# Optimization experiments

Measured on AMD Instinct MI355X. Metric: run time of the kernel, lower is better.

The kernel has to match this reference:

```python
import jax, jax.numpy as jnp
import numpy as np

TAU = 2.0         # LIFNode default tau
VTH = 1.0         # v_threshold
ALPHA = 2.0       # ATan surrogate alpha
TIME_STEP = 4     # hard-coded in RecurrentLIFNode
NUM_LAYERS = 4
HIDDEN = 512
INPUT = 512
T, B = 128, 512

@jax.custom_vjp
def atan_spike(x):
    # heaviside forward, ATan surrogate backward (spikingjelly surrogate.ATan)
    return (x >= 0.0).astype(x.dtype)

def _atan_fwd(x):
    return atan_spike(x), x

def _atan_bwd(x, g):
    return (g * (ALPHA / 2.0) / (1.0 + (jnp.pi / 2.0 * ALPHA * x) ** 2),)

atan_spike.defvjp(_atan_fwd, _atan_bwd)

def lif_burst(v, inp):
    # run one LIFCell time_step times with fixed input `inp`, accumulate averages
    acc_v = jnp.zeros_like(v)
    acc_s = jnp.zeros_like(v)
    for _ in range(TIME_STEP):
        v = v + (inp - v) / TAU          # neuronal_charge (decay_input=True, v_reset=None)
        s = atan_spike(v - VTH)          # neuronal_fire
        v = v - s * VTH                  # soft reset (v_reset=None)
        acc_v = acc_v + v
        acc_s = acc_s + s
    return v, acc_v / TIME_STEP, acc_s / TIME_STEP


def setup_inputs() -> dict:
    key = jax.random.key(0)
    k1, k2, k3 = jax.random.split(key, 3)
    x = jax.random.normal(k1, (T, B, INPUT), dtype=jnp.float32)
    bound = 1.0 / np.sqrt(INPUT)
    W = jax.random.uniform(k2, (HIDDEN, INPUT), dtype=jnp.float32, minval=-bound, maxval=bound)
    b = jax.random.uniform(k3, (HIDDEN,), dtype=jnp.float32, minval=-bound, maxval=bound)
    return {"x": x, "W": W, "b": b}


def reference(x, W, b):
    # x: [T, B, input]; project once (linear_ih)
    xp = jnp.einsum('tbi,hi->tbh', x, W) + b   # [T, B, H]
    Bsz, H = x.shape[1], W.shape[0]
    init_state = jnp.zeros((NUM_LAYERS, Bsz, H), dtype=x.dtype)  # current_state persists across t

    def step(cur, xt):
        curs = [cur[i] for i in range(NUM_LAYERS)]
        y = xt
        new_vs = []
        last_spk = None
        for i in range(NUM_LAYERS):
            curs[i], avg_v, avg_s = lif_burst(curs[i], y)
            new_vs.append(avg_v)
            y = avg_v          # next layer consumes averaged membrane state
            last_spk = avg_s
        return jnp.stack(curs), (last_spk, jnp.stack(new_vs))

    _, (out, states_seq) = jax.lax.scan(step, init_state, xp)
    # out: [T, B, H] averaged spikes of last layer; final new_states_list: [L, B, H]
    return out, states_seq[-1]
```

## Files before the change

kernel.cpp:

```cpp
#include <hip/hip_runtime.h>
#include <stdint.h>

#define TT 128
#define BSZ 512
#define HID 512
#define KDIM 512
#define BH (BSZ*HID)

__global__ __launch_bounds__(256) void gemm_f32(
    const float* __restrict__ A, const float* __restrict__ W,
    const float* __restrict__ bias, float* __restrict__ C) {
  __shared__ float As[2][16][132];
  __shared__ float Bs[2][16][132];
  const int t  = threadIdx.x;
  const int m0 = blockIdx.y * 128;
  const int n0 = blockIdx.x * 128;
  const int tx = t & 15;
  const int ty = t >> 4;
  const int r0 = t >> 2;
  const int kg = t & 3;

  float acc[8][8];
  #pragma unroll
  for (int i = 0; i < 8; ++i)
    #pragma unroll
    for (int j = 0; j < 8; ++j) acc[i][j] = 0.f;

  const float* Ap = A + (size_t)(m0 + r0) * KDIM + kg * 4;
  const float* Wp = W + (size_t)(n0 + r0) * KDIM + kg * 4;

  float4 a0 = *(const float4*)Ap;
  float4 w0 = *(const float4*)Wp;
  float4 a1 = *(const float4*)(Ap + (size_t)64 * KDIM);
  float4 w1 = *(const float4*)(Wp + (size_t)64 * KDIM);

  #define STAGE(BUF) do { \
    As[BUF][kg*4+0][r0]    = a0.x; As[BUF][kg*4+1][r0]    = a0.y; \
    As[BUF][kg*4+2][r0]    = a0.z; As[BUF][kg*4+3][r0]    = a0.w; \
    Bs[BUF][kg*4+0][r0]    = w0.x; Bs[BUF][kg*4+1][r0]    = w0.y; \
    Bs[BUF][kg*4+2][r0]    = w0.z; Bs[BUF][kg*4+3][r0]    = w0.w; \
    As[BUF][kg*4+0][r0+64] = a1.x; As[BUF][kg*4+1][r0+64] = a1.y; \
    As[BUF][kg*4+2][r0+64] = a1.z; As[BUF][kg*4+3][r0+64] = a1.w; \
    Bs[BUF][kg*4+0][r0+64] = w1.x; Bs[BUF][kg*4+1][r0+64] = w1.y; \
    Bs[BUF][kg*4+2][r0+64] = w1.z; Bs[BUF][kg*4+3][r0+64] = w1.w; \
  } while (0)

  STAGE(0);

  int cur = 0;
  for (int k0 = 0; k0 < KDIM; k0 += 16) {
    __syncthreads();
    const bool more = (k0 + 16 < KDIM);
    if (more) {
      a0 = *(const float4*)(Ap + k0 + 16);
      w0 = *(const float4*)(Wp + k0 + 16);
      a1 = *(const float4*)(Ap + (size_t)64 * KDIM + k0 + 16);
      w1 = *(const float4*)(Wp + (size_t)64 * KDIM + k0 + 16);
    }

    #pragma unroll
    for (int kk = 0; kk < 16; ++kk) {
      const float4 xa0 = *(const float4*)&As[cur][kk][ty*8];
      const float4 xa1 = *(const float4*)&As[cur][kk][ty*8 + 4];
      const float4 xb0 = *(const float4*)&Bs[cur][kk][tx*4];
      const float4 xb1 = *(const float4*)&Bs[cur][kk][64 + tx*4];
      const float a[8] = {xa0.x,xa0.y,xa0.z,xa0.w,xa1.x,xa1.y,xa1.z,xa1.w};
      const float b[8] = {xb0.x,xb0.y,xb0.z,xb0.w,xb1.x,xb1.y,xb1.z,xb1.w};
      #pragma unroll
      for (int i = 0; i < 8; ++i)
        #pragma unroll
        for (int j = 0; j < 8; ++j)
          acc[i][j] = __builtin_fmaf(a[i], b[j], acc[i][j]);
    }

    if (more) {
      const int nb = cur ^ 1;
      STAGE(nb);
    }
    cur ^= 1;
  }
  #undef STAGE

  const float4 bv0 = *(const float4*)&bias[n0 + tx*4];
  const float4 bv1 = *(const float4*)&bias[n0 + 64 + tx*4];
  #pragma unroll
  for (int i = 0; i < 8; ++i) {
    const float4 v0 = {acc[i][0] + bv0.x, acc[i][1] + bv0.y, acc[i][2] + bv0.z, acc[i][3] + bv0.w};
    const float4 v1 = {acc[i][4] + bv1.x, acc[i][5] + bv1.y, acc[i][6] + bv1.z, acc[i][7] + bv1.w};
    float* cp = C + (size_t)(m0 + ty*8 + i) * HID + n0;
    *(float4*)(cp + tx*4)      = v0;
    *(float4*)(cp + 64 + tx*4) = v1;
  }
}

__device__ __forceinline__ float lif_step(float y, float v[4], float av[4]) {
  float as3 = 0.f;
  #pragma unroll
  for (int l = 0; l < 4; ++l) {
    float vv = v[l];
    float accv = 0.f, accs = 0.f;
    #pragma unroll
    for (int k = 0; k < 4; ++k) {
      const float d = y - vv;
      vv = __builtin_fmaf(d, 0.5f, vv);
      const float spk = (vv >= 1.0f) ? 1.0f : 0.0f;
      vv -= spk;
      accv += vv;
      accs += spk;
    }
    v[l] = vv;
    const float a = accv * 0.25f;
    av[l] = a;
    y = a;
    as3 = accs;
  }
  return as3;
}

__global__ __launch_bounds__(256) void lif_scan(
    const float* __restrict__ xp, float* __restrict__ outp, float* __restrict__ vstate,
    int tc, int first, int last) {
  const int idx = blockIdx.x * 256 + threadIdx.x;
  float v[4];
  if (first) {
    #pragma unroll
    for (int l = 0; l < 4; ++l) v[l] = 0.f;
  } else {
    #pragma unroll
    for (int l = 0; l < 4; ++l) v[l] = vstate[(size_t)l * BH + idx];
  }
  float av[4] = {0.f, 0.f, 0.f, 0.f};
  const float* p = xp + idx;
  float* op = outp + idx;

  if ((tc & 3) == 0 && tc >= 8) {
    float curb[4];
    #pragma unroll
    for (int i = 0; i < 4; ++i) curb[i] = p[(size_t)i * BH];
    for (int t = 0; t + 4 < tc; t += 4) {
      float nxtb[4];
      #pragma unroll
      for (int i = 0; i < 4; ++i) nxtb[i] = p[(size_t)(i + 4) * BH];
      #pragma unroll
      for (int i = 0; i < 4; ++i) {
        const float as3 = lif_step(curb[i], v, av);
        op[(size_t)i * BH] = as3 * 0.25f;
      }
      #pragma unroll
      for (int i = 0; i < 4; ++i) curb[i] = nxtb[i];
      p += 4 * BH; op += 4 * BH;
    }
    #pragma unroll
    for (int i = 0; i < 4; ++i) {
      const float as3 = lif_step(curb[i], v, av);
      op[(size_t)i * BH] = as3 * 0.25f;
    }
  } else {
    for (int t = 0; t < tc; ++t) {
      const float as3 = lif_step(p[0], v, av);
      *op = as3 * 0.25f;
      p += BH; op += BH;
    }
  }

  if (last) {
    #pragma unroll
    for (int l = 0; l < 4; ++l) vstate[(size_t)l * BH + idx] = av[l];
  } else {
    #pragma unroll
    for (int l = 0; l < 4; ++l) vstate[(size_t)l * BH + idx] = v[l];
  }
}

extern "C" void kernel_launch(void* const* d_in, const int* in_sizes, int n_in,
                              void* d_out, int out_size, void* d_ws, size_t ws_size,
                              hipStream_t stream) {
  const float* x = (const float*)d_in[0];
  const float* W = (const float*)d_in[1];
  const float* b = (const float*)d_in[2];
  float* out    = (float*)d_out;
  float* states = out + (size_t)TT * BH;

  int tc = TT;
  while (tc > 1 && (size_t)tc * BH * 4ull > ws_size) tc >>= 1;
  float* xp = (float*)d_ws;
  const int nc = TT / tc;

  for (int c = 0; c < nc; ++c) {
    hipLaunchKernelGGL(gemm_f32, dim3(HID / 128, tc * BSZ / 128), dim3(256), 0, stream,
                       x + (size_t)c * tc * BH, W, b, xp);
    hipLaunchKernelGGL(lif_scan, dim3(BH / 256), dim3(256), 0, stream,
                       xp, out + (size_t)c * tc * BH, states,
                       tc, c == 0 ? 1 : 0, c == nc - 1 ? 1 : 0);
  }
}
```

Baseline: 615.9 us.

## Enlarge GEMM tile to 256x128 and process two elements per thread in LIF scan

The FP32 GEMM tile grows from 128x128 to 256x128, so each thread computes a 16x8 accumulator block, with four A rows staged per thread and launch bounds raised to two blocks per CU. This raises arithmetic intensity per shared-memory load and halves the grid. The LIF scan now handles two neighbouring elements per thread using float2 loads and stores, which gives each thread two independent dependency chains to interleave. The cost is much higher register pressure in the GEMM (128 accumulators), which could spill or reduce occupancy, and half as many threads in the scan.

After: 710.0 us. 15.3% more time.

```diff
diff --git a/kernel.cpp b/kernel.cpp
--- a/kernel.cpp
+++ b/kernel.cpp
@@ -7,45 +7,56 @@
 #define KDIM 512
 #define BH (BSZ*HID)
 
-__global__ __launch_bounds__(256) void gemm_f32(
+__global__ __launch_bounds__(256, 2) void gemm_f32(
     const float* __restrict__ A, const float* __restrict__ W,
     const float* __restrict__ bias, float* __restrict__ C) {
-  __shared__ float As[2][16][132];
+  __shared__ float As[2][16][260];
   __shared__ float Bs[2][16][132];
   const int t  = threadIdx.x;
-  const int m0 = blockIdx.y * 128;
+  const int m0 = blockIdx.y * 256;
   const int n0 = blockIdx.x * 128;
   const int tx = t & 15;
   const int ty = t >> 4;
   const int r0 = t >> 2;
-  const int kg = t & 3;
-
-  float acc[8][8];
+  const int kg4 = (t & 3) * 4;
+
+  float4 acc0[16], acc1[16];
   #pragma unroll
-  for (int i = 0; i < 8; ++i)
-    #pragma unroll
-    for (int j = 0; j < 8; ++j) acc[i][j] = 0.f;
-
-  const float* Ap = A + (size_t)(m0 + r0) * KDIM + kg * 4;
-  const float* Wp = W + (size_t)(n0 + r0) * KDIM + kg * 4;
+  for (int i = 0; i < 16; ++i) {
+    acc0[i] = (float4){0.f,0.f,0.f,0.f};
+    acc1[i] = (float4){0.f,0.f,0.f,0.f};
+  }
+
+  const float* Ap = A + (size_t)(m0 + r0) * KDIM + kg4;
+  const float* Wp = W + (size_t)(n0 + r0) * KDIM + kg4;
 
   float4 a0 = *(const float4*)Ap;
+  float4 a1 = *(const float4*)(Ap + (size_t)64  * KDIM);
+  float4 a2 = *(const float4*)(Ap + (size_t)128 * KDIM);
+  float4 a3 = *(const float4*)(Ap + (size_t)192 * KDIM);
   float4 w0 = *(const float4*)Wp;
-  float4 a1 = *(const float4*)(Ap + (size_t)64 * KDIM);
   float4 w1 = *(const float4*)(Wp + (size_t)64 * KDIM);
 
   #define STAGE(BUF) do { \
-    As[BUF][kg*4+0][r0]    = a0.x; As[BUF][kg*4+1][r0]    = a0.y; \
-    As[BUF][kg*4+2][r0]    = a0.z; As[BUF][kg*4+3][r0]    = a0.w; \
-    Bs[BUF][kg*4+0][r0]    = w0.x; Bs[BUF][kg*4+1][r0]    = w0.y; \
-    Bs[BUF][kg*4+2][r0]    = w0.z; Bs[BUF][kg*4+3][r0]    = w0.w; \
-    As[BUF][kg*4+0][r0+64] = a1.x; As[BUF][kg*4+1][r0+64] = a1.y; \
-    As[BUF][kg*4+2][r0+64] = a1.z; As[BUF][kg*4+3][r0+64] = a1.w; \
-    Bs[BUF][kg*4+0][r0+64] = w1.x; Bs[BUF][kg*4+1][r0+64] = w1.y; \
-    Bs[BUF][kg*4+2][r0+64] = w1.z; Bs[BUF][kg*4+3][r0+64] = w1.w; \
+    As[BUF][kg4+0][r0]     = a0.x; As[BUF][kg4+1][r0]     = a0.y; As[BUF][kg4+2][r0]     = a0.z; As[BUF][kg4+3][r0]     = a0.w; \
+    As[BUF][kg4+0][r0+64]  = a1.x; As[BUF][kg4+1][r0+64]  = a1.y; As[BUF][kg4+2][r0+64]  = a1.z; As[BUF][kg4+3][r0+64]  = a1.w; \
+    As[BUF][kg4+0][r0+128] = a2.x; As[BUF][kg4+1][r0+128] = a2.y; As[BUF][kg4+2][r0+128] = a2.z; As[BUF][kg4+3][r0+128] = a2.w; \
+    As[BUF][kg4+0][r0+192] = a3.x; As[BUF][kg4+1][r0+192] = a3.y; As[BUF][kg4+2][r0+192] = a3.z; As[BUF][kg4+3][r0+192] = a3.w; \
+    Bs[BUF][kg4+0][r0]     = w0.x; Bs[BUF][kg4+1][r0]     = w0.y; Bs[BUF][kg4+2][r0]     = w0.z; Bs[BUF][kg4+3][r0]     = w0.w; \
+    Bs[BUF][kg4+0][r0+64]  = w1.x; Bs[BUF][kg4+1][r0+64]  = w1.y; Bs[BUF][kg4+2][r0+64]  = w1.z; Bs[BUF][kg4+3][r0+64]  = w1.w; \
   } while (0)
 
   STAGE(0);
+
+  #define FMA8(AV, I) \
+    acc0[I].x = __builtin_fmaf(AV, bf0.x, acc0[I].x); \
+    acc0[I].y = __builtin_fmaf(AV, bf0.y, acc0[I].y); \
+    acc0[I].z = __builtin_fmaf(AV, bf0.z, acc0[I].z); \
+    acc0[I].w = __builtin_fmaf(AV, bf0.w, acc0[I].w); \
+    acc1[I].x = __builtin_fmaf(AV, bf1.x, acc1[I].x); \
+    acc1[I].y = __builtin_fmaf(AV, bf1.y, acc1[I].y); \
+    acc1[I].z = __builtin_fmaf(AV, bf1.z, acc1[I].z); \
+    acc1[I].w = __builtin_fmaf(AV, bf1.w, acc1[I].w);
 
   int cur = 0;
   for (int k0 = 0; k0 < KDIM; k0 += 16) {
@@ -53,41 +64,40 @@
     const bool more = (k0 + 16 < KDIM);
     if (more) {
       a0 = *(const float4*)(Ap + k0 + 16);
+      a1 = *(const float4*)(Ap + (size_t)64  * KDIM + k0 + 16);
+      a2 = *(const float4*)(Ap + (size_t)128 * KDIM + k0 + 16);
+      a3 = *(const float4*)(Ap + (size_t)192 * KDIM + k0 + 16);
       w0 = *(const float4*)(Wp + k0 + 16);
-      a1 = *(const float4*)(Ap + (size_t)64 * KDIM + k0 + 16);
       w1 = *(const float4*)(Wp + (size_t)64 * KDIM + k0 + 16);
     }
 
     #pragma unroll
     for (int kk = 0; kk < 16; ++kk) {
-      const float4 xa0 = *(const float4*)&As[cur][kk][ty*8];
-      const float4 xa1 = *(const float4*)&As[cur][kk][ty*8 + 4];
-      const float4 xb0 = *(const float4*)&Bs[cur][kk][tx*4];
-      const float4 xb1 = *(const float4*)&Bs[cur][kk][64 + tx*4];
-      const float a[8] = {xa0.x,xa0.y,xa0.z,xa0.w,xa1.x,xa1.y,xa1.z,xa1.w};
-      const float b[8] = {xb0.x,xb0.y,xb0.z,xb0.w,xb1.x,xb1.y,xb1.z,xb1.w};
-      #pragma unroll
-      for (int i = 0; i < 8; ++i)
-        #pragma unroll
-        for (int j = 0; j < 8; ++j)
-          acc[i][j] = __builtin_fmaf(a[i], b[j], acc[i][j]);
-    }
-
-    if (more) {
-      const int nb = cur ^ 1;
-      STAGE(nb);
-    }
+      const float4 bf0 = *(const float4*)&Bs[cur][kk][tx*4];
+      const float4 bf1 = *(const float4*)&Bs[cur][kk][64 + tx*4];
+      const float4 af0 = *(const float4*)&As[cur][kk][ty*16];
+      const float4 af1 = *(const float4*)&As[cur][kk][ty*16 + 4];
+      const float4 af2 = *(const float4*)&As[cur][kk][ty*16 + 8];
+      const float4 af3 = *(const float4*)&As[cur][kk][ty*16 + 12];
+      FMA8(af0.x, 0)  FMA8(af0.y, 1)  FMA8(af0.z, 2)  FMA8(af0.w, 3)
+      FMA8(af1.x, 4)  FMA8(af1.y, 5)  FMA8(af1.z, 6)  FMA8(af1.w, 7)
+      FMA8(af2.x, 8)  FMA8(af2.y, 9)  FMA8(af2.z, 10) FMA8(af2.w, 11)
+      FMA8(af3.x, 12) FMA8(af3.y, 13) FMA8(af3.z, 14) FMA8(af3.w, 15)
+    }
+
+    if (more) STAGE(cur ^ 1);
     cur ^= 1;
   }
   #undef STAGE
+  #undef FMA8
 
   const float4 bv0 = *(const float4*)&bias[n0 + tx*4];
   const float4 bv1 = *(const float4*)&bias[n0 + 64 + tx*4];
   #pragma unroll
-  for (int i = 0; i < 8; ++i) {
-    const float4 v0 = {acc[i][0] + bv0.x, acc[i][1] + bv0.y, acc[i][2] + bv0.z, acc[i][3] + bv0.w};
-    const float4 v1 = {acc[i][4] + bv1.x, acc[i][5] + bv1.y, acc[i][6] + bv1.z, acc[i][7] + bv1.w};
-    float* cp = C + (size_t)(m0 + ty*8 + i) * HID + n0;
+  for (int i = 0; i < 16; ++i) {
+    const float4 v0 = {acc0[i].x + bv0.x, acc0[i].y + bv0.y, acc0[i].z + bv0.z, acc0[i].w + bv0.w};
+    const float4 v1 = {acc1[i].x + bv1.x, acc1[i].y + bv1.y, acc1[i].z + bv1.z, acc1[i].w + bv1.w};
+    float* cp = C + (size_t)(m0 + ty*16 + i) * HID + n0;
     *(float4*)(cp + tx*4)      = v0;
     *(float4*)(cp + 64 + tx*4) = v1;
   }
@@ -120,55 +130,65 @@
 __global__ __launch_bounds__(256) void lif_scan(
     const float* __restrict__ xp, float* __restrict__ outp, float* __restrict__ vstate,
     int tc, int first, int last) {
-  const int idx = blockIdx.x * 256 + threadIdx.x;
-  float v[4];
+  const int gid = blockIdx.x * 256 + threadIdx.x;
+  const int S2 = BH / 2;
+  const float2* p = (const float2*)xp + gid;
+  float2* op = (float2*)outp + gid;
+  float2* vs = (float2*)vstate;
+
+  float v0[4], v1[4];
   if (first) {
     #pragma unroll
-    for (int l = 0; l < 4; ++l) v[l] = 0.f;
+    for (int l = 0; l < 4; ++l) { v0[l] = 0.f; v1[l] = 0.f; }
   } else {
     #pragma unroll
-    for (int l = 0; l < 4; ++l) v[l] = vstate[(size_t)l * BH + idx];
-  }
-  float av[4] = {0.f, 0.f, 0.f, 0.f};
-  const float* p = xp + idx;
-  float* op = outp + idx;
+    for (int l = 0; l < 4; ++l) {
+      const float2 vv = vs[(size_t)l * S2 + gid];
+      v0[l] = vv.x; v1[l] = vv.y;
+    }
+  }
+  float av0[4] = {0.f,0.f,0.f,0.f}, av1[4] = {0.f,0.f,0.f,0.f};
 
   if ((tc & 3) == 0 && tc >= 8) {
-    float curb[4];
-    #pragma unroll
-    for (int i = 0; i < 4; ++i) curb[i] = p[(size_t)i * BH];
+    float2 curb[4];
+    #pragma unroll
+    for (int i = 0; i < 4; ++i) curb[i] = p[(size_t)i * S2];
     for (int t = 0; t + 4 < tc; t += 4) {
-      float nxtb[4];
+      float2 nxt[4];
       #pragma unroll
-      for (int i = 0; i < 4; ++i) nxtb[i] = p[(size_t)(i + 4) * BH];
+      for (int i = 0; i < 4; ++i) nxt[i] = p[(size_t)(i + 4) * S2];
       #pragma unroll
       for (int i = 0; i < 4; ++i) {
-        const float as3 = lif_step(curb[i], v, av);
-        op[(size_t)i * BH] = as3 * 0.25f;
+        const float s0 = lif_step(curb[i].x, v0, av0);
+        const float s1 = lif_step(curb[i].y, v1, av1);
+        op[(size_t)i * S2] = (float2){s0 * 0.25f, s1 * 0.25f};
       }
       #pragma unroll
-      for (int i = 0; i < 4; ++i) curb[i] = nxtb[i];
-      p += 4 * BH; op += 4 * BH;
+      for (int i = 0; i < 4; ++i) curb[i] = nxt[i];
+      p += (size_t)4 * S2; op += (size_t)4 * S2;
     }
     #pragma unroll
     for (int i = 0; i < 4; ++i) {
-      const float as3 = lif_step(curb[i], v, av);
-      op[(size_t)i * BH] = as3 * 0.25f;
+      const float s0 = lif_step(curb[i].x, v0, av0);
+      const float s1 = lif_step(curb[i].y, v1, av1);
+      op[(size_t)i * S2] = (float2){s0 * 0.25f, s1 * 0.25f};
     }
   } else {
     for (int t = 0; t < tc; ++t) {
-      const float as3 = lif_step(p[0], v, av);
-      *op = as3 * 0.25f;
-      p += BH; op += BH;
+      const float2 cv = *p;
+      const float s0 = lif_step(cv.x, v0, av0);
+      const float s1 = lif_step(cv.y, v1, av1);
+      *op = (float2){s0 * 0.25f, s1 * 0.25f};
+      p += S2; op += S2;
     }
   }
 
   if (last) {
     #pragma unroll
-    for (int l = 0; l < 4; ++l) vstate[(size_t)l * BH + idx] = av[l];
+    for (int l = 0; l < 4; ++l) vs[(size_t)l * S2 + gid] = (float2){av0[l], av1[l]};
   } else {
     #pragma unroll
-    for (int l = 0; l < 4; ++l) vstate[(size_t)l * BH + idx] = v[l];
+    for (int l = 0; l < 4; ++l) vs[(size_t)l * S2 + gid] = (float2){v0[l], v1[l]};
   }
 }
 
@@ -187,9 +207,9 @@
   const int nc = TT / tc;
 
   for (int c = 0; c < nc; ++c) {
-    hipLaunchKernelGGL(gemm_f32, dim3(HID / 128, tc * BSZ / 128), dim3(256), 0, stream,
+    hipLaunchKernelGGL(gemm_f32, dim3(HID / 128, tc * BSZ / 256), dim3(256), 0, stream,
                        x + (size_t)c * tc * BH, W, b, xp);
-    hipLaunchKernelGGL(lif_scan, dim3(BH / 256), dim3(256), 0, stream,
+    hipLaunchKernelGGL(lif_scan, dim3(BH / 512), dim3(256), 0, stream,
                        xp, out + (size_t)c * tc * BH, states,
                        tc, c == 0 ? 1 : 0, c == nc - 1 ? 1 : 0);
   }
```
